# Performance work log

Hardware: AMD Instinct MI355X
Metric: run time of the kernel (lower is better)

Reference implementation:

```python
import jax, jax.numpy as jnp
import numpy as np

EPS = 1e-6

def _ln(x, g, b):
    m = jnp.mean(x, -1, keepdims=True)
    v = jnp.mean((x - m) ** 2, -1, keepdims=True)
    return (x - m) * jax.lax.rsqrt(v + 1e-5) * g + b

def _mha(qin, kin, vin, wq, bq, wk, bk, wv, bv, wo, bo, nh=8):
    B, T, D = qin.shape
    S = kin.shape[1]
    dh = D // nh
    q = (qin @ wq + bq).reshape(B, T, nh, dh)
    k = (kin @ wk + bk).reshape(B, S, nh, dh)
    v = (vin @ wv + bv).reshape(B, S, nh, dh)
    a = jax.nn.softmax(jnp.einsum('bthd,bshd->bhts', q, k) / np.float32(np.sqrt(dh)), -1)
    o = jnp.einsum('bhts,bshd->bthd', a, v).reshape(B, T, D)
    return o @ wo + bo

def _sinu_pe(pos, num_feats=128, temperature=20.0):
    # pos: [..., 2] (x, y); returns [..., 2*num_feats] ordered (y-feats, x-feats)
    dim_t = temperature ** ((2 * (jnp.arange(num_feats) // 2)) / num_feats)
    e = pos[..., None] * (2 * np.pi) / dim_t  # [..., 2, F]
    e = jnp.stack([jnp.sin(e[..., 0::2]), jnp.cos(e[..., 1::2])], -1).reshape(e.shape)
    return jnp.concatenate([e[..., 1, :], e[..., 0, :]], -1)

def _spatial36(b1, b2, sizes):
    # b1, b2: [B, Q, 4]; sizes: [B, 2] = (h, w). UPT-style 18 feats + log -> 36.
    h = sizes[:, 0:1]; w = sizes[:, 1:2]
    c1x = (b1[..., 0] + b1[..., 2]) / 2; c1y = (b1[..., 1] + b1[..., 3]) / 2
    c2x = (b2[..., 0] + b2[..., 2]) / 2; c2y = (b2[..., 1] + b2[..., 3]) / 2
    w1 = b1[..., 2] - b1[..., 0]; h1 = b1[..., 3] - b1[..., 1]
    w2 = b2[..., 2] - b2[..., 0]; h2 = b2[..., 3] - b2[..., 1]
    a1 = w1 * h1; a2 = w2 * h2
    dx = jnp.abs(c2x - c1x) / (w1 + EPS)
    dy = jnp.abs(c2y - c1y) / (h1 + EPS)
    ix = jnp.clip(jnp.minimum(b1[..., 2], b2[..., 2]) - jnp.maximum(b1[..., 0], b2[..., 0]), 0)
    iy = jnp.clip(jnp.minimum(b1[..., 3], b2[..., 3]) - jnp.maximum(b1[..., 1], b2[..., 1]), 0)
    inter = ix * iy
    iou = inter / (a1 + a2 - inter + EPS)
    f = jnp.stack([c1x / w, c1y / h, c2x / w, c2y / h, w1 / w, h1 / h, w2 / w, h2 / h,
                   a1 / (h * w), a2 / (h * w), a2 / (a1 + EPS), w1 / (h1 + EPS), w2 / (h2 + EPS), iou,
                   (c2x > c1x) * dx, (c2x < c1x) * dx, (c2y > c1y) * dy, (c2y < c1y) * dy], -1)
    return jnp.concatenate([f, jnp.log(f + EPS)], -1)

def _forward(boxes, embeds, image_sizes, pose, line, sw1, sb1, sw2, sb2, sw3, sb3, bw, bb, pw, pb, lw, lb, enc_pe_w, enc_pe_b, enc_qkv_w, enc_qkv_b, enc_out_w, enc_out_b, enc_ff1_w, enc_ff1_b, enc_ff2_w, enc_ff2_b, enc_ln1_g, enc_ln1_b, enc_ln2_g, enc_ln2_b, dec_q_w, dec_q_b, dec_kv_w, dec_kv_b, dec_out_w, dec_out_b, dec_ff1_w, dec_ff1_b, dec_ff2_w, dec_ff2_b, dec_ln1_g, dec_ln1_b, dec_ln2_g, dec_ln2_b, fc1_w, fc1_b, fc2_w, fc2_b, mln1_g, mln1_b, mln2_g, mln2_b, m1_w, m1_b, m2_w, m2_b, labels, nh):
    B, N, _ = boxes.shape
    # static human-object pairing (x != y) & (x < nh)
    xg, yg = np.meshgrid(np.arange(N), np.arange(N), indexing='ij')
    keep = (xg != yg) & (xg < nh)
    xk = jnp.asarray(xg[keep]); yk = jnp.asarray(yg[keep])  # [P]
    # line features: adaptive-avg-pool(1,1) + 1x1 conv == spatial mean + linear
    line_feat = jnp.mean(line, axis=(2, 3)) @ lw + lb  # [B, 256]
    # spatial head on all N*N ordered pairs, then gather kept pairs
    xa = jnp.asarray(xg.reshape(-1)); ya = jnp.asarray(yg.reshape(-1))
    f36 = _spatial36(boxes[:, xa], boxes[:, ya], image_sizes)  # [B, N*N, 36]
    s = jax.nn.relu(f36 @ sw1 + sb1)
    s = jax.nn.relu(s @ sw2 + sb2)
    s = jax.nn.relu(s @ sw3 + sb3)
    spa = s.reshape(B, N, N, -1)[:, xk, yk]  # [B, P, R]
    # box sinusoidal positional encodings (cat of centre-PE and wh-PE)
    whwh = image_sizes[:, jnp.array([1, 0, 1, 0])][:, None]  # [B,1,4]
    bxn = boxes / whwh
    ctr = (bxn[..., :2] + bxn[..., 2:]) / 2
    whb = bxn[..., 2:] - bxn[..., :2]
    box_pe = jnp.concatenate([_sinu_pe(ctr), _sinu_pe(whb)], -1)  # [B, N, 512]
    # 2-layer transformer encoder over instance tokens (pos added to q,k)
    posx = box_pe @ enc_pe_w + enc_pe_b
    x = embeds
    for i in range(enc_qkv_w.shape[0]):
        wq, wk_, wv = jnp.split(enc_qkv_w[i], 3, axis=1)
        bq, bk_, bv = jnp.split(enc_qkv_b[i], 3)
        qk = x + posx
        att = _mha(qk, qk, x, wq, bq, wk_, bk_, wv, bv, enc_out_w[i], enc_out_b[i])
        x = _ln(x + att, enc_ln1_g[i], enc_ln1_b[i])
        ff = jax.nn.relu(x @ enc_ff1_w[i] + enc_ff1_b[i]) @ enc_ff2_w[i] + enc_ff2_b[i]
        x = _ln(x + ff, enc_ln2_g[i], enc_ln2_b[i])
    # pair gather + human/object positional embeds (box PE projected + line feature)
    pe_h = box_pe[:, xk] @ bw + bb + line_feat[:, None, :]
    pe_o = box_pe[:, yk] @ bw + bb + line_feat[:, None, :]
    h = x[:, xk]; o = x[:, yk]  # [B, P, 256]
    pose_ctx = pose @ pw + pb  # [B, M, 256]
    # HO refine decoder: cross-attention from pair tokens to pose tokens
    for l in range(dec_q_w.shape[0]):
        wk_, wv = jnp.split(dec_kv_w[l], 2, axis=1)
        bk_, bv = jnp.split(dec_kv_b[l], 2)
        def _layer(feat, pe):
            att = _mha(feat + pe, pose_ctx, pose_ctx, dec_q_w[l], dec_q_b[l], wk_, bk_, wv, bv, dec_out_w[l], dec_out_b[l])
            feat = _ln(feat + att, dec_ln1_g[l], dec_ln1_b[l])
            ff = jax.nn.relu(feat @ dec_ff1_w[l] + dec_ff1_b[l]) @ dec_ff2_w[l] + dec_ff2_b[l]
            return _ln(feat + ff, dec_ln2_g[l], dec_ln2_b[l])
        h = _layer(h, pe_h)
        o = _layer(o, pe_o)
    # multi-modal fusion
    ho = jnp.concatenate([h, o], -1)  # [B, P, 512]
    ho = _ln(ho @ fc1_w + fc1_b, mln1_g, mln1_b)
    sp = _ln(spa @ fc2_w + fc2_b, mln2_g, mln2_b)
    z = jax.nn.relu(jnp.concatenate([ho, sp], -1))
    z = jax.nn.relu(z @ m1_w + m1_b)
    z = jax.nn.relu(z @ m2_w + m2_b)
    return z  # [B, P, 256] HOI query features

def setup_inputs() -> dict:
    key = jax.random.key(0)
    ks = iter(jax.random.split(key, 80))
    B, N, NH, M, HH, WW = 16, 128, 32, 64, 8, 8
    W = 0.05
    def rn(shape, s=1.0):
        return jax.random.normal(next(ks), shape, dtype=jnp.float32) * s
    def ru(shape):
        return jax.random.uniform(next(ks), shape, dtype=jnp.float32)
    sizes = 800.0 + 480.0 * ru((B, 2))  # (h, w)
    wh = sizes[:, jnp.array([1, 0])]
    xy = ru((B, N, 2)) * wh[:, None] * 0.7
    bwh = ru((B, N, 2)) * wh[:, None] * 0.25 + 4.0
    boxes = jnp.concatenate([xy, xy + bwh], -1)
    labels = jnp.concatenate([jnp.zeros((B, NH), jnp.int32), jax.random.randint(next(ks), (B, N - NH), 1, 81, dtype=jnp.int32)], -1)
    return dict(
        boxes=boxes, embeds=rn((B, N, 256)), image_sizes=sizes, pose=rn((B, M, 768)), line=rn((B, 2048, HH, WW)),
        sw1=rn((36, 128), W), sb1=jnp.zeros((128,)), sw2=rn((128, 256), W), sb2=jnp.zeros((256,)), sw3=rn((256, 256), W), sb3=jnp.zeros((256,)),
        bw=rn((512, 256), W), bb=jnp.zeros((256,)), pw=rn((768, 256), W), pb=jnp.zeros((256,)), lw=rn((2048, 256), W), lb=jnp.zeros((256,)),
        enc_pe_w=rn((512, 256), W), enc_pe_b=jnp.zeros((256,)),
        enc_qkv_w=rn((2, 256, 768), W), enc_qkv_b=jnp.zeros((2, 768)), enc_out_w=rn((2, 256, 256), W), enc_out_b=jnp.zeros((2, 256)),
        enc_ff1_w=rn((2, 256, 1024), W), enc_ff1_b=jnp.zeros((2, 1024)), enc_ff2_w=rn((2, 1024, 256), W), enc_ff2_b=jnp.zeros((2, 256)),
        enc_ln1_g=jnp.ones((2, 256)), enc_ln1_b=jnp.zeros((2, 256)), enc_ln2_g=jnp.ones((2, 256)), enc_ln2_b=jnp.zeros((2, 256)),
        dec_q_w=rn((2, 256, 256), W), dec_q_b=jnp.zeros((2, 256)), dec_kv_w=rn((2, 256, 512), W), dec_kv_b=jnp.zeros((2, 512)),
        dec_out_w=rn((2, 256, 256), W), dec_out_b=jnp.zeros((2, 256)),
        dec_ff1_w=rn((2, 256, 1024), W), dec_ff1_b=jnp.zeros((2, 1024)), dec_ff2_w=rn((2, 1024, 256), W), dec_ff2_b=jnp.zeros((2, 256)),
        dec_ln1_g=jnp.ones((2, 256)), dec_ln1_b=jnp.zeros((2, 256)), dec_ln2_g=jnp.ones((2, 256)), dec_ln2_b=jnp.zeros((2, 256)),
        fc1_w=rn((512, 256), W), fc1_b=jnp.zeros((256,)), fc2_w=rn((256, 256), W), fc2_b=jnp.zeros((256,)),
        mln1_g=jnp.ones((256,)), mln1_b=jnp.zeros((256,)), mln2_g=jnp.ones((256,)), mln2_b=jnp.zeros((256,)),
        m1_w=rn((512, 384), W), m1_b=jnp.zeros((384,)), m2_w=rn((384, 256), W), m2_b=jnp.zeros((256,)),
        labels=labels, nh=NH)

def reference(boxes, embeds, image_sizes, pose, line, sw1, sb1, sw2, sb2, sw3, sb3, bw, bb, pw, pb, lw, lb, enc_pe_w, enc_pe_b, enc_qkv_w, enc_qkv_b, enc_out_w, enc_out_b, enc_ff1_w, enc_ff1_b, enc_ff2_w, enc_ff2_b, enc_ln1_g, enc_ln1_b, enc_ln2_g, enc_ln2_b, dec_q_w, dec_q_b, dec_kv_w, dec_kv_b, dec_out_w, dec_out_b, dec_ff1_w, dec_ff1_b, dec_ff2_w, dec_ff2_b, dec_ln1_g, dec_ln1_b, dec_ln2_g, dec_ln2_b, fc1_w, fc1_b, fc2_w, fc2_b, mln1_g, mln1_b, mln2_g, mln2_b, m1_w, m1_b, m2_w, m2_b, labels, nh):
    return _forward(boxes, embeds, image_sizes, pose, line, sw1, sb1, sw2, sb2, sw3, sb3, bw, bb, pw, pb, lw, lb, enc_pe_w, enc_pe_b, enc_qkv_w, enc_qkv_b, enc_out_w, enc_out_b, enc_ff1_w, enc_ff1_b, enc_ff2_w, enc_ff2_b, enc_ln1_g, enc_ln1_b, enc_ln2_g, enc_ln2_b, dec_q_w, dec_q_b, dec_kv_w, dec_kv_b, dec_out_w, dec_out_b, dec_ff1_w, dec_ff1_b, dec_ff2_w, dec_ff2_b, dec_ln1_g, dec_ln1_b, dec_ln2_g, dec_ln2_b, fc1_w, fc1_b, fc2_w, fc2_b, mln1_g, mln1_b, mln2_g, mln2_b, m1_w, m1_b, m2_w, m2_b, labels, nh)
```

## Files before the change

kernel.cpp:

```cpp
#include <hip/hip_runtime.h>
#include <stdint.h>

static constexpr int B      = 16;
static constexpr int N      = 128;
static constexpr int P      = 4064;
static constexpr int MPOSE  = 64;
static constexpr int64_t BN = (int64_t)B * N;
static constexpr int64_t BP = (int64_t)B * P;

#define TWO_PI 6.283185307179586f
#define QSCALE 0.17677669529663687f

typedef __attribute__((ext_vector_type(4))) float f32x4;
typedef __attribute__((ext_vector_type(8))) short bf16x8;
typedef __attribute__((ext_vector_type(8))) unsigned short u16x8;
typedef __attribute__((ext_vector_type(4))) unsigned short u16x4;

__device__ __forceinline__ unsigned short f2bf(float f) {
    union { float f; unsigned u; } v; v.f = f;
    unsigned r = (v.u + 0x7fffu + ((v.u >> 16) & 1u)) >> 16;
    return (unsigned short)r;
}
__device__ __forceinline__ float bf2f(unsigned short u) {
    union { unsigned u; float f; } v; v.u = (unsigned)u << 16;
    return v.f;
}
__device__ __forceinline__ void pair_xy(int p, int& x, int& y) {
    x = p / 127;
    int r = p - x * 127;
    y = (r < x) ? r : r + 1;
}
__device__ __forceinline__ int xcd_swz(int orig, int nwg) {
    int q = nwg >> 3, r = nwg & 7;
    int xcd = orig & 7, idx = orig >> 3;
    return (xcd < r ? xcd * (q + 1) : r * (q + 1) + (xcd - r) * q) + idx;
}
__device__ __forceinline__ void gld16(const unsigned short* g, unsigned short* l) {
    __builtin_amdgcn_global_load_lds(
        (const __attribute__((address_space(1))) void*)g,
        (__attribute__((address_space(3))) void*)l, 16, 0, 0);
}

struct WDesc { const float* src; int64_t dstOff; int K, Nn, Kpad, blockStart; };
struct WTable { WDesc d[29]; int nDesc; };

__global__ __launch_bounds__(256) void wprep_all_k(WTable t, unsigned short* __restrict__ wt)
{
    __shared__ float s[32][33];
    int bid = blockIdx.x;
    int di = 0;
    for (int i = 1; i < t.nDesc; ++i) if (t.d[i].blockStart <= bid) di = i;
    const WDesc& d = t.d[di];
    int lbid = bid - d.blockStart;
    int kTiles = d.Kpad >> 5;
    int k0 = (lbid % kTiles) * 32, n0 = (lbid / kTiles) * 32;
    int tx = threadIdx.x & 31, ty = threadIdx.x >> 5;
#pragma unroll
    for (int i = 0; i < 4; ++i) {
        int k = k0 + ty + i * 8;
        s[ty + i * 8][tx] = (k < d.K) ? d.src[(int64_t)k * d.Nn + n0 + tx] : 0.f;
    }
    __syncthreads();
    unsigned short* dst = wt + d.dstOff;
#pragma unroll
    for (int i = 0; i < 4; ++i) {
        int n = n0 + ty + i * 8;
        dst[(int64_t)n * d.Kpad + k0 + tx] = f2bf(s[tx][ty + i * 8]);
    }
}

template <bool RELU_OUT>
__global__ __launch_bounds__(256) void bgemm_k(
    const float* __restrict__ A, const float* __restrict__ A2, int lda,
    const unsigned short* __restrict__ Bt, int ldk,
    const float* __restrict__ bias,
    const float* __restrict__ Cadd, int addStride, int addCols,
    const float* __restrict__ lfp,
    float* __restrict__ C, int ldc,
    int kSteps)
{
    __shared__ unsigned short As[128][40];
    __shared__ unsigned short Bs[128][40];
    const int tid  = threadIdx.x;
    const int lane = tid & 63;
    const int wave = tid >> 6;
    const int wr = wave >> 1, wc = wave & 1;
    const int row0 = blockIdx.y * 128, col0 = blockIdx.x * 128;
    const int l15 = lane & 15, l4 = lane >> 4;
    const int sr = tid >> 1;
    const int sh = (tid & 1) * 16;

    f32x4 acc[4][4] = {};

    for (int ks = 0; ks < kSteps; ++ks) {
        const int k0 = ks * 32;
        {
            const int64_t off = (int64_t)(row0 + sr) * lda + k0 + sh;
            const float* ap = A + off;
            float v[16];
#pragma unroll
            for (int i = 0; i < 4; ++i) {
                float4 tv = ((const float4*)ap)[i];
                v[i*4+0] = tv.x; v[i*4+1] = tv.y; v[i*4+2] = tv.z; v[i*4+3] = tv.w;
            }
            if (A2) {
                const float* ap2 = A2 + off;
#pragma unroll
                for (int i = 0; i < 4; ++i) {
                    float4 tv = ((const float4*)ap2)[i];
                    v[i*4+0] += tv.x; v[i*4+1] += tv.y; v[i*4+2] += tv.z; v[i*4+3] += tv.w;
                }
            }
            u16x8 p0, p1;
#pragma unroll
            for (int j = 0; j < 8; ++j) { p0[j] = f2bf(v[j]); p1[j] = f2bf(v[8 + j]); }
            *(u16x8*)&As[sr][sh]     = p0;
            *(u16x8*)&As[sr][sh + 8] = p1;
        }
        {
            const unsigned short* bp = Bt + (int64_t)(col0 + sr) * ldk + k0 + sh;
            *(u16x8*)&Bs[sr][sh]     = *(const u16x8*)bp;
            *(u16x8*)&Bs[sr][sh + 8] = *(const u16x8*)(bp + 8);
        }
        __syncthreads();
        bf16x8 af[4], bfr[4];
#pragma unroll
        for (int f = 0; f < 4; ++f) {
            af[f]  = *(const bf16x8*)&As[wr * 64 + f * 16 + l15][l4 * 8];
            bfr[f] = *(const bf16x8*)&Bs[wc * 64 + f * 16 + l15][l4 * 8];
        }
#pragma unroll
        for (int i = 0; i < 4; ++i)
#pragma unroll
            for (int j = 0; j < 4; ++j)
                acc[i][j] = __builtin_amdgcn_mfma_f32_16x16x32_bf16(af[i], bfr[j], acc[i][j], 0, 0, 0);
        __syncthreads();
    }
#pragma unroll
    for (int i = 0; i < 4; ++i) {
        int rb = row0 + wr * 64 + i * 16 + l4 * 4;
#pragma unroll
        for (int j = 0; j < 4; ++j) {
            int c = col0 + wc * 64 + j * 16 + l15;
            float bv = bias ? bias[c] : 0.f;
#pragma unroll
            for (int e = 0; e < 4; ++e) {
                int r = rb + e;
                float vv = acc[i][j][e] + bv;
                if (Cadd && c < addCols) vv += Cadd[(int64_t)r * addStride + c];
                if (lfp) vv += lfp[(r >> 7) * 256 + c];
                if (RELU_OUT) vv = fmaxf(vv, 0.f);
                C[(int64_t)r * ldc + c] = vv;
            }
        }
    }
}

static void bgemm(hipStream_t st,
                  const float* A, const float* A2, int lda,
                  const unsigned short* Bt, int ldk, const float* bias,
                  const float* Cadd, int addStride, int addCols, const float* lfp,
                  float* C, int ldc, int M, int Ncols, int K, bool reluOut)
{
    dim3 g(Ncols / 128, M / 128), b(256);
    if (reluOut) bgemm_k<true><<<g,b,0,st>>>(A,A2,lda,Bt,ldk,bias,Cadd,addStride,addCols,lfp,C,ldc,K/32);
    else         bgemm_k<false><<<g,b,0,st>>>(A,A2,lda,Bt,ldk,bias,Cadd,addStride,addCols,lfp,C,ldc,K/32);
}

__global__ __launch_bounds__(256) void tgemm16_k(
    const float* __restrict__ A, int lda,
    const unsigned short* __restrict__ Bt, int ldk,
    const float* __restrict__ bias,
    const float* __restrict__ res,
    const float* __restrict__ g, const float* __restrict__ be,
    float* __restrict__ C, int kSteps)
{
    __shared__ unsigned short As[16][40];
    __shared__ unsigned short Bs[256][40];
    __shared__ float partS[16][4], partQ[16][4];
    __shared__ float statM[16], statI[16];
    const int tid = threadIdx.x;
    const int lane = tid & 63, w = tid >> 6;
    const int l15 = lane & 15, l4 = lane >> 4;
    const int row0 = blockIdx.x * 16;

    f32x4 acc[4] = {};
    for (int ks = 0; ks < kSteps; ++ks) {
        int k0 = ks * 32;
        if (tid < 64) {
            const float* ap = A + (int64_t)(row0 + (tid >> 2)) * lda + k0 + (tid & 3) * 8;
            float4 t0 = ((const float4*)ap)[0];
            float4 t1 = ((const float4*)ap)[1];
            u16x8 p;
            p[0]=f2bf(t0.x); p[1]=f2bf(t0.y); p[2]=f2bf(t0.z); p[3]=f2bf(t0.w);
            p[4]=f2bf(t1.x); p[5]=f2bf(t1.y); p[6]=f2bf(t1.z); p[7]=f2bf(t1.w);
            *(u16x8*)&As[tid >> 2][(tid & 3) * 8] = p;
        }
        {
            const unsigned short* bp = Bt + (int64_t)tid * ldk + k0;
#pragma unroll
            for (int q = 0; q < 4; ++q)
                *(u16x8*)&Bs[tid][q * 8] = *(const u16x8*)(bp + q * 8);
        }
        __syncthreads();
        bf16x8 af = *(const bf16x8*)&As[l15][l4 * 8];
        bf16x8 bfr[4];
#pragma unroll
        for (int f = 0; f < 4; ++f)
            bfr[f] = *(const bf16x8*)&Bs[w * 64 + f * 16 + l15][l4 * 8];
#pragma unroll
        for (int j = 0; j < 4; ++j)
            acc[j] = __builtin_amdgcn_mfma_f32_16x16x32_bf16(af, bfr[j], acc[j], 0, 0, 0);
        __syncthreads();
    }
    float ps[4] = {}, pq[4] = {};
#pragma unroll
    for (int j = 0; j < 4; ++j) {
        int c = w * 64 + j * 16 + l15;
#pragma unroll
        for (int e = 0; e < 4; ++e) {
            int r = l4 * 4 + e;
            float v = acc[j][e] + bias[c] + res[(int64_t)(row0 + r) * 256 + c];
            acc[j][e] = v;
            ps[e] += v;
            pq[e] += v * v;
        }
    }
#pragma unroll
    for (int e = 0; e < 4; ++e) {
#pragma unroll
        for (int m = 1; m < 16; m <<= 1) {
            ps[e] += __shfl_xor(ps[e], m);
            pq[e] += __shfl_xor(pq[e], m);
        }
    }
    if (l15 == 0) {
#pragma unroll
        for (int e = 0; e < 4; ++e) {
            int r = l4 * 4 + e;
            partS[r][w] = ps[e];
            partQ[r][w] = pq[e];
        }
    }
    __syncthreads();
    if (tid < 16) {
        float s = partS[tid][0] + partS[tid][1] + partS[tid][2] + partS[tid][3];
        float q = partQ[tid][0] + partQ[tid][1] + partQ[tid][2] + partQ[tid][3];
        float m = s * (1.f/256.f);
        float var = q * (1.f/256.f) - m * m;
        statM[tid] = m;
        statI[tid] = rsqrtf(var + 1e-5f);
    }
    __syncthreads();
#pragma unroll
    for (int j = 0; j < 4; ++j) {
        int c = w * 64 + j * 16 + l15;
#pragma unroll
        for (int e = 0; e < 4; ++e) {
            int r = l4 * 4 + e;
            C[(int64_t)(row0 + r) * 256 + c] = (acc[j][e] - statM[r]) * statI[r] * g[c] + be[c];
        }
    }
}

template <bool RELU_OUT, bool OUT_BF16>
__global__ __launch_bounds__(256) void hgemm_k(
    const unsigned short* __restrict__ A, int lda,
    const unsigned short* __restrict__ Bt, int ldk,
    const float* __restrict__ bias,
    void* __restrict__ Cv, int ldc,
    int kSteps, int nx)
{
    __shared__ unsigned short As[128][32];
    __shared__ unsigned short Bs[128][32];
    const int tid  = threadIdx.x;
    const int lane = tid & 63;
    const int wave = tid >> 6;
    const int wr = wave >> 1, wc = wave & 1;
    const int wgid = xcd_swz(blockIdx.x, gridDim.x);
    const int row0 = (wgid / nx) * 128, col0 = (wgid % nx) * 128;
    const int l15 = lane & 15, l4 = lane >> 4;
    const int srow = lane >> 2;
    const int scol = (lane & 3) * 8;

    f32x4 acc[4][4] = {};
    for (int ks = 0; ks < kSteps; ++ks) {
        const int k0 = ks * 32;
#pragma unroll
        for (int i = 0; i < 2; ++i) {
            int seg = wave * 2 + i;
            int r = seg * 16 + srow;
            gld16(A  + (int64_t)(row0 + r) * lda + k0 + scol, &As[seg * 16][0]);
            gld16(Bt + (int64_t)(col0 + r) * ldk + k0 + scol, &Bs[seg * 16][0]);
        }
        __syncthreads();
        bf16x8 af[4], bfr[4];
#pragma unroll
        for (int f = 0; f < 4; ++f) {
            af[f]  = *(const bf16x8*)&As[wr * 64 + f * 16 + l15][l4 * 8];
            bfr[f] = *(const bf16x8*)&Bs[wc * 64 + f * 16 + l15][l4 * 8];
        }
#pragma unroll
        for (int i = 0; i < 4; ++i)
#pragma unroll
            for (int j = 0; j < 4; ++j)
                acc[i][j] = __builtin_amdgcn_mfma_f32_16x16x32_bf16(af[i], bfr[j], acc[i][j], 0, 0, 0);
        __syncthreads();
    }
#pragma unroll
    for (int i = 0; i < 4; ++i) {
        int rb = row0 + wr * 64 + i * 16 + l4 * 4;
#pragma unroll
        for (int j = 0; j < 4; ++j) {
            int c = col0 + wc * 64 + j * 16 + l15;
            float bv = bias ? bias[c] : 0.f;
#pragma unroll
            for (int e = 0; e < 4; ++e) {
                int64_t off = (int64_t)(rb + e) * ldc + c;
                float vv = acc[i][j][e] + bv;
                if (RELU_OUT) vv = fmaxf(vv, 0.f);
                if (OUT_BF16) ((unsigned short*)Cv)[off] = f2bf(vv);
                else          ((float*)Cv)[off] = vv;
            }
        }
    }
}

__global__ __launch_bounds__(256) void spa_k(
    const float* __restrict__ boxes, const float* __restrict__ sizes,
    const unsigned short* __restrict__ W1, const float* __restrict__ b1,
    const unsigned short* __restrict__ W2, const float* __restrict__ b2,
    unsigned short* __restrict__ t3out, int chunk0)
{
    __shared__ unsigned short F[128][72];
    __shared__ unsigned short Bs[128][40];
    __shared__ unsigned short D1s[128][136];
    const int tid  = threadIdx.x;
    const int lane = tid & 63;
    const int wave = tid >> 6;
    const int wr = wave >> 1, wc = wave & 1;
    const int row0 = blockIdx.x * 128;
    const int l15 = lane & 15, l4 = lane >> 4;
    const int sr = tid >> 1;
    const int sh = (tid & 1) * 16;

    if (tid < 128) {
        int gp = chunk0 + row0 + tid;
        int b = gp / P, p = gp - b * P;
        int xi, yi; pair_xy(p, xi, yi);
        const float* b1x = boxes + ((int64_t)b * N + xi) * 4;
        const float* b2x = boxes + ((int64_t)b * N + yi) * 4;
        float h = sizes[b * 2 + 0], w = sizes[b * 2 + 1];
        float c1x = (b1x[0] + b1x[2]) * 0.5f, c1y = (b1x[1] + b1x[3]) * 0.5f;
        float c2x = (b2x[0] + b2x[2]) * 0.5f, c2y = (b2x[1] + b2x[3]) * 0.5f;
        float w1 = b1x[2] - b1x[0], h1 = b1x[3] - b1x[1];
        float w2 = b2x[2] - b2x[0], h2 = b2x[3] - b2x[1];
        float a1 = w1 * h1, a2 = w2 * h2;
        float dx = fabsf(c2x - c1x) / (w1 + 1e-6f);
        float dy = fabsf(c2y - c1y) / (h1 + 1e-6f);
        float ix = fmaxf(fminf(b1x[2], b2x[2]) - fmaxf(b1x[0], b2x[0]), 0.f);
        float iy = fmaxf(fminf(b1x[3], b2x[3]) - fmaxf(b1x[1], b2x[1]), 0.f);
        float inter = ix * iy;
        float iou = inter / (a1 + a2 - inter + 1e-6f);
        float f[18];
        f[0] = c1x / w;  f[1] = c1y / h;  f[2] = c2x / w;  f[3] = c2y / h;
        f[4] = w1 / w;   f[5] = h1 / h;   f[6] = w2 / w;   f[7] = h2 / h;
        f[8] = a1 / (h * w); f[9] = a2 / (h * w); f[10] = a2 / (a1 + 1e-6f);
        f[11] = w1 / (h1 + 1e-6f); f[12] = w2 / (h2 + 1e-6f); f[13] = iou;
        f[14] = (c2x > c1x) ? dx : 0.f;  f[15] = (c2x < c1x) ? dx : 0.f;
        f[16] = (c2y > c1y) ? dy : 0.f;  f[17] = (c2y < c1y) ? dy : 0.f;
#pragma unroll
        for (int i = 0; i < 18; ++i) {
            F[tid][i]      = f2bf(f[i]);
            F[tid][18 + i] = f2bf(logf(f[i] + 1e-6f));
        }
#pragma unroll
        for (int i = 36; i < 64; ++i) F[tid][i] = 0;
    }
    __syncthreads();

    f32x4 acc1[4][4] = {};
    for (int ks = 0; ks < 2; ++ks) {
        const int k0 = ks * 32;
        {
            const unsigned short* bp = W1 + (int64_t)sr * 64 + k0 + sh;
            *(u16x8*)&Bs[sr][sh]     = *(const u16x8*)bp;
            *(u16x8*)&Bs[sr][sh + 8] = *(const u16x8*)(bp + 8);
        }
        __syncthreads();
        bf16x8 af[4], bfr[4];
#pragma unroll
        for (int f = 0; f < 4; ++f) {
            af[f]  = *(const bf16x8*)&F[wr * 64 + f * 16 + l15][k0 + l4 * 8];
            bfr[f] = *(const bf16x8*)&Bs[wc * 64 + f * 16 + l15][l4 * 8];
        }
#pragma unroll
        for (int i = 0; i < 4; ++i)
#pragma unroll
            for (int j = 0; j < 4; ++j)
                acc1[i][j] = __builtin_amdgcn_mfma_f32_16x16x32_bf16(af[i], bfr[j], acc1[i][j], 0, 0, 0);
        __syncthreads();
    }
#pragma unroll
    for (int i = 0; i < 4; ++i) {
        int rb = wr * 64 + i * 16 + l4 * 4;
#pragma unroll
        for (int j = 0; j < 4; ++j) {
            int c = wc * 64 + j * 16 + l15;
            float bv = b1[c];
#pragma unroll
            for (int e = 0; e < 4; ++e)
                D1s[rb + e][c] = f2bf(fmaxf(acc1[i][j][e] + bv, 0.f));
        }
    }
    __syncthreads();

    f32x4 acc2[2][4][4] = {};
#pragma unroll
    for (int n = 0; n < 2; ++n) {
        for (int kk = 0; kk < 4; ++kk) {
            {
                const unsigned short* bp = W2 + (int64_t)(n * 128 + sr) * 128 + kk * 32 + sh;
                *(u16x8*)&Bs[sr][sh]     = *(const u16x8*)bp;
                *(u16x8*)&Bs[sr][sh + 8] = *(const u16x8*)(bp + 8);
            }
            __syncthreads();
            bf16x8 af[4], bfr[4];
#pragma unroll
            for (int f = 0; f < 4; ++f) {
                af[f]  = *(const bf16x8*)&D1s[wr * 64 + f * 16 + l15][kk * 32 + l4 * 8];
                bfr[f] = *(const bf16x8*)&Bs[wc * 64 + f * 16 + l15][l4 * 8];
            }
#pragma unroll
            for (int i = 0; i < 4; ++i)
#pragma unroll
                for (int j = 0; j < 4; ++j)
                    acc2[n][i][j] = __builtin_amdgcn_mfma_f32_16x16x32_bf16(af[i], bfr[j], acc2[n][i][j], 0, 0, 0);
            __syncthreads();
        }
    }
#pragma unroll
    for (int n = 0; n < 2; ++n)
#pragma unroll
    for (int i = 0; i < 4; ++i) {
        int rb = row0 + wr * 64 + i * 16 + l4 * 4;
#pragma unroll
        for (int j = 0; j < 4; ++j) {
            int c = n * 128 + wc * 64 + j * 16 + l15;
            float bv = b2[c];
#pragma unroll
            for (int e = 0; e < 4; ++e)
                t3out[(int64_t)(rb + e) * 256 + c] = f2bf(fmaxf(acc2[n][i][j][e] + bv, 0.f));
        }
    }
}

__global__ __launch_bounds__(256) void zprep_k(
    const float* __restrict__ UV, const float* __restrict__ fb,
    const unsigned short* __restrict__ t3,
    const float* __restrict__ g1, const float* __restrict__ be1,
    const float* __restrict__ g2, const float* __restrict__ be2,
    unsigned short* __restrict__ zb, int chunk0, int rows)
{
    int wave = threadIdx.x >> 6, lane = threadIdx.x & 63;
    int li = blockIdx.x * 4 + wave;
    if (li >= rows) return;
    int gp = chunk0 + li;
    int b = gp / P, p = gp - b * P;
    int xi, yi; pair_xy(p, xi, yi);
    int c = lane * 4;
    {
        float4 u  = *(const float4*)(UV + ((int64_t)(b * 128 + xi)) * 512 + c);
        float4 vv = *(const float4*)(UV + ((int64_t)(b * 128 + yi)) * 512 + 256 + c);
        float4 fbv = *(const float4*)(fb + c);
        float4 v;
        v.x = u.x + vv.x + fbv.x; v.y = u.y + vv.y + fbv.y;
        v.z = u.z + vv.z + fbv.z; v.w = u.w + vv.w + fbv.w;
        float s  = v.x + v.y + v.z + v.w;
        float sq = v.x*v.x + v.y*v.y + v.z*v.z + v.w*v.w;
#pragma unroll
        for (int off = 1; off < 64; off <<= 1) {
            s  += __shfl_xor(s, off);
            sq += __shfl_xor(sq, off);
        }
        float m = s * (1.f/256.f);
        float var = sq * (1.f/256.f) - m * m;
        float inv = rsqrtf(var + 1e-5f);
        float4 gg = *(const float4*)(g1 + c);
        float4 bb = *(const float4*)(be1 + c);
        u16x4 o;
        o[0] = f2bf(fmaxf((v.x - m) * inv * gg.x + bb.x, 0.f));
        o[1] = f2bf(fmaxf((v.y - m) * inv * gg.y + bb.y, 0.f));
        o[2] = f2bf(fmaxf((v.z - m) * inv * gg.z + bb.z, 0.f));
        o[3] = f2bf(fmaxf((v.w - m) * inv * gg.w + bb.w, 0.f));
        *(u16x4*)(zb + (int64_t)li * 512 + c) = o;
    }
    {
        u16x4 u = *(const u16x4*)(t3 + (int64_t)li * 256 + c);
        float4 v;
        v.x = bf2f(u[0]); v.y = bf2f(u[1]); v.z = bf2f(u[2]); v.w = bf2f(u[3]);
        float s  = v.x + v.y + v.z + v.w;
        float sq = v.x*v.x + v.y*v.y + v.z*v.z + v.w*v.w;
#pragma unroll
        for (int off = 1; off < 64; off <<= 1) {
            s  += __shfl_xor(s, off);
            sq += __shfl_xor(sq, off);
        }
        float m = s * (1.f/256.f);
        float var = sq * (1.f/256.f) - m * m;
        float inv = rsqrtf(var + 1e-5f);
        float4 gg = *(const float4*)(g2 + c);
        float4 bb = *(const float4*)(be2 + c);
        u16x4 o;
        o[0] = f2bf(fmaxf((v.x - m) * inv * gg.x + bb.x, 0.f));
        o[1] = f2bf(fmaxf((v.y - m) * inv * gg.y + bb.y, 0.f));
        o[2] = f2bf(fmaxf((v.z - m) * inv * gg.z + bb.z, 0.f));
        o[3] = f2bf(fmaxf((v.w - m) * inv * gg.w + bb.w, 0.f));
        *(u16x4*)(zb + (int64_t)li * 512 + 256 + c) = o;
    }
}

__global__ __launch_bounds__(256) void line_mean_k(const float* __restrict__ line, float* __restrict__ lm)
{
    int wave = threadIdx.x >> 6, lane = threadIdx.x & 63;
    int bc = blockIdx.x * 4 + wave;
    float v = line[(int64_t)bc * 64 + lane];
#pragma unroll
    for (int off = 1; off < 64; off <<= 1) v += __shfl_xor(v, off);
    if (lane == 0) lm[bc] = v * (1.f/64.f);
}

__global__ __launch_bounds__(256) void line_proj_k(
    const float* __restrict__ lm, const float* __restrict__ lw,
    const float* __restrict__ lb, float* __restrict__ lf)
{
    __shared__ float red[8][32];
    int b = blockIdx.y, jg = blockIdx.x;
    int jj = threadIdx.x & 31, cc = threadIdx.x >> 5;
    int j = jg * 32 + jj;
    const float* lmb = lm + (int64_t)b * 2048 + cc * 256;
    const float* lwp = lw + (int64_t)(cc * 256) * 256 + j;
    float acc = 0.f;
#pragma unroll 4
    for (int k = 0; k < 256; ++k) acc += lmb[k] * lwp[(int64_t)k * 256];
    red[cc][jj] = acc;
    __syncthreads();
    if (cc == 0) {
        float s = lb[j];
#pragma unroll
        for (int i = 0; i < 8; ++i) s += red[i][jj];
        lf[b * 256 + j] = s;
    }
}

__global__ __launch_bounds__(512) void boxpe_k(
    const float* __restrict__ boxes, const float* __restrict__ sizes, float* __restrict__ boxpe)
{
    int row = blockIdx.x;
    int b = row >> 7;
    int i = threadIdx.x;
    const float* bx = boxes + (int64_t)row * 4;
    float h = sizes[b * 2 + 0], w = sizes[b * 2 + 1];
    float x0 = bx[0] / w, y0 = bx[1] / h, x1 = bx[2] / w, y1 = bx[3] / h;
    int seg = i >> 7, j = i & 127, k = j >> 1;
    float val;
    switch (seg) {
        case 0: val = (y0 + y1) * 0.5f; break;
        case 1: val = (x0 + x1) * 0.5f; break;
        case 2: val = (y1 - y0); break;
        default: val = (x1 - x0); break;
    }
    float dimt = exp2f((float)k * (4.321928094887362f / 64.f));
    float arg = val * TWO_PI / dimt;
    boxpe[(int64_t)row * 512 + i] = (j & 1) ? cosf(arg) : sinf(arg);
}

__global__ __launch_bounds__(128) void enc_attn_k(
    const float* __restrict__ qkv, float* __restrict__ outp)
{
    int b = blockIdx.x >> 3, hd = blockIdx.x & 7;
    __shared__ float kl[128][32];
    __shared__ float vl[128][32];
    int tid = threadIdx.x;
    for (int i = tid; i < 128 * 32; i += 128) {
        int s = i >> 5, j = i & 31;
        const float* rp = qkv + ((int64_t)(b * 128 + s)) * 768 + hd * 32 + j;
        kl[s][j] = rp[256];
        vl[s][j] = rp[512];
    }
    __syncthreads();
    int t = tid;
    const float* qp = qkv + ((int64_t)(b * 128 + t)) * 768 + hd * 32;
    float qr[32];
#pragma unroll
    for (int j = 0; j < 32; ++j) qr[j] = qp[j] * QSCALE;
    float m = -1e30f, l = 0.f;
    for (int s = 0; s < 128; ++s) {
        float d = 0.f;
#pragma unroll
        for (int j = 0; j < 32; ++j) d += qr[j] * kl[s][j];
        float mn = fmaxf(m, d);
        l = l * __expf(m - mn) + __expf(d - mn);
        m = mn;
    }
    float acc[32] = {};
    for (int s = 0; s < 128; ++s) {
        float d = 0.f;
#pragma unroll
        for (int j = 0; j < 32; ++j) d += qr[j] * kl[s][j];
        float wgt = __expf(d - m);
#pragma unroll
        for (int j = 0; j < 32; ++j) acc[j] += wgt * vl[s][j];
    }
    float linv = 1.f / l;
    float* op = outp + ((int64_t)(b * 128 + t)) * 256 + hd * 32;
#pragma unroll
    for (int j = 0; j < 32; ++j) op[j] = acc[j] * linv;
}

__global__ __launch_bounds__(256) void dec_attn_k(
    const float* __restrict__ q, const float* __restrict__ kv, int ldkv,
    float* __restrict__ outp, int rows, int rpb)
{
    int hd = blockIdx.y;
    int r0 = blockIdx.x * 256;
    __shared__ float kl[2][64][32];
    __shared__ float vl[2][64][32];
    int tid = threadIdx.x;
    int b0 = r0 / rpb;
    int b1 = (r0 + 255) / rpb;
    if (b1 >= B) b1 = B - 1;
    for (int i = tid; i < 64 * 32; i += 256) {
        int s = i >> 5, j = i & 31;
        int64_t off0 = ((int64_t)(b0 * MPOSE + s)) * ldkv + hd * 32 + j;
        int64_t off1 = ((int64_t)(b1 * MPOSE + s)) * ldkv + hd * 32 + j;
        kl[0][s][j] = kv[off0];
        vl[0][s][j] = kv[off0 + 256];
        kl[1][s][j] = kv[off1];
        vl[1][s][j] = kv[off1 + 256];
    }
    __syncthreads();
    int r = r0 + tid;
    if (r >= rows) return;
    int which = (r / rpb == b0) ? 0 : 1;
    int64_t qoff = (int64_t)r * 256 + hd * 32;
    float qr[32];
#pragma unroll
    for (int j = 0; j < 32; ++j) qr[j] = q[qoff + j] * QSCALE;
    float m = -1e30f, l = 0.f;
    for (int s = 0; s < 64; ++s) {
        float d = 0.f;
#pragma unroll
        for (int j = 0; j < 32; ++j) d += qr[j] * kl[which][s][j];
        float mn = fmaxf(m, d);
        l = l * __expf(m - mn) + __expf(d - mn);
        m = mn;
    }
    float acc[32] = {};
    for (int s = 0; s < 64; ++s) {
        float d = 0.f;
#pragma unroll
        for (int j = 0; j < 32; ++j) d += qr[j] * kl[which][s][j];
        float wgt = __expf(d - m);
#pragma unroll
        for (int j = 0; j < 32; ++j) acc[j] += wgt * vl[which][s][j];
    }
    float linv = 1.f / l;
#pragma unroll
    for (int j = 0; j < 32; ++j) outp[qoff + j] = acc[j] * linv;
}

static constexpr int64_t WT_QKV  = 0;
static constexpr int64_t WT_EOUT = WT_QKV  + 2*196608;
static constexpr int64_t WT_EFF1 = WT_EOUT + 2*65536;
static constexpr int64_t WT_EFF2 = WT_EFF1 + 2*262144;
static constexpr int64_t WT_DQ   = WT_EFF2 + 2*262144;
static constexpr int64_t WT_DKV  = WT_DQ   + 2*65536;
static constexpr int64_t WT_DOUT = WT_DKV  + 2*131072;
static constexpr int64_t WT_DFF1 = WT_DOUT + 2*65536;
static constexpr int64_t WT_DFF2 = WT_DFF1 + 2*262144;
static constexpr int64_t WT_SW1  = WT_DFF2 + 2*262144;
static constexpr int64_t WT_SW2  = WT_SW1 + 8192;
static constexpr int64_t WT_SW3  = WT_SW2 + 32768;
static constexpr int64_t WT_BW   = WT_SW3 + 65536;
static constexpr int64_t WT_PW   = WT_BW  + 131072;
static constexpr int64_t WT_EPE  = WT_PW  + 196608;
static constexpr int64_t WT_FC1  = WT_EPE + 131072;
static constexpr int64_t WT_FC2  = WT_FC1 + 131072;
static constexpr int64_t WT_M1   = WT_FC2 + 65536;
static constexpr int64_t WT_M2   = WT_M1  + 196608;
static constexpr int64_t WT_TOTAL = WT_M2 + 98304;

extern "C" void kernel_launch(void* const* d_in, const int* in_sizes, int n_in,
                              void* d_out, int out_size, void* d_ws, size_t ws_size,
                              hipStream_t stream)
{
    (void)in_sizes; (void)n_in; (void)out_size;
    const float* boxes     = (const float*)d_in[0];
    const float* embeds    = (const float*)d_in[1];
    const float* sizes     = (const float*)d_in[2];
    const float* pose      = (const float*)d_in[3];
    const float* line      = (const float*)d_in[4];
    const float* sw1 = (const float*)d_in[5];  const float* sb1 = (const float*)d_in[6];
    const float* sw2 = (const float*)d_in[7];  const float* sb2 = (const float*)d_in[8];
    const float* sw3 = (const float*)d_in[9];  const float* sb3 = (const float*)d_in[10];
    const float* bw  = (const float*)d_in[11]; const float* bb  = (const float*)d_in[12];
    const float* pw  = (const float*)d_in[13]; const float* pb  = (const float*)d_in[14];
    const float* lw  = (const float*)d_in[15]; const float* lb  = (const float*)d_in[16];
    const float* enc_pe_w  = (const float*)d_in[17]; const float* enc_pe_b = (const float*)d_in[18];
    const float* enc_qkv_w = (const float*)d_in[19]; const float* enc_qkv_b = (const float*)d_in[20];
    const float* enc_out_w = (const float*)d_in[21]; const float* enc_out_b = (const float*)d_in[22];
    const float* enc_ff1_w = (const float*)d_in[23]; const float* enc_ff1_b = (const float*)d_in[24];
    const float* enc_ff2_w = (const float*)d_in[25]; const float* enc_ff2_b = (const float*)d_in[26];
    const float* enc_ln1_g = (const float*)d_in[27]; const float* enc_ln1_b = (const float*)d_in[28];
    const float* enc_ln2_g = (const float*)d_in[29]; const float* enc_ln2_b = (const float*)d_in[30];
    const float* dec_q_w   = (const float*)d_in[31]; const float* dec_q_b  = (const float*)d_in[32];
    const float* dec_kv_w  = (const float*)d_in[33]; const float* dec_kv_b = (const float*)d_in[34];
    const float* dec_out_w = (const float*)d_in[35]; const float* dec_out_b = (const float*)d_in[36];
    const float* dec_ff1_w = (const float*)d_in[37]; const float* dec_ff1_b = (const float*)d_in[38];
    const float* dec_ff2_w = (const float*)d_in[39]; const float* dec_ff2_b = (const float*)d_in[40];
    const float* dec_ln1_g = (const float*)d_in[41]; const float* dec_ln1_b = (const float*)d_in[42];
    const float* dec_ln2_g = (const float*)d_in[43]; const float* dec_ln2_b = (const float*)d_in[44];
    const float* fc1_w = (const float*)d_in[45]; const float* fc1_b = (const float*)d_in[46];
    const float* fc2_w = (const float*)d_in[47]; const float* fc2_b = (const float*)d_in[48];
    const float* mln1_g = (const float*)d_in[49]; const float* mln1_b = (const float*)d_in[50];
    const float* mln2_g = (const float*)d_in[51]; const float* mln2_b = (const float*)d_in[52];
    const float* m1_w = (const float*)d_in[53]; const float* m1_b = (const float*)d_in[54];
    const float* m2_w = (const float*)d_in[55]; const float* m2_b = (const float*)d_in[56];
    float* out = (float*)d_out;

    float* base = (float*)d_ws;
    int64_t wsf = (int64_t)(ws_size / sizeof(float));
    float* x_   = base;
    float* bpw_ = x_   + 524288;
    float* lf   = bpw_ + 524288;
    float* kv0  = lf   + 4096;
    unsigned short* wt = (unsigned short*)(kv0 + 1048576);
    float* arena = (float*)(wt + WT_TOTAL);
    const int64_t LIVE_F = arena - base;
    int64_t arena_f = wsf - LIVE_F;
    if (arena_f < 0) arena_f = 0;

    float* posx  = arena;
    float* boxpe = posx  + 524288;
    float* pqkv  = boxpe + 1048576;
    float* e_qkv = pqkv  + 3145728;
    float* e_t   = e_qkv + 1572864;
    float* e_ff  = e_t   + 524288;
    float* pctx  = e_ff  + 2097152;
    float* lm    = pctx  + 262144;

    int64_t rc = ((arena_f * 2) / 1152) & ~127LL;
    if (rc > BP) rc = BP;
    if (rc < 128) rc = 128;

    {
        WTable T;
        int nd = 0, bs = 0;
        auto add = [&](const float* src, int64_t dstOff, int K, int Nn, int Kpad) {
            T.d[nd] = { src, dstOff, K, Nn, Kpad, bs };
            bs += (Kpad / 32) * (Nn / 32);
            ++nd;
        };
        for (int i = 0; i < 2; ++i) {
            add(enc_qkv_w + (int64_t)i*196608, WT_QKV  + i*196608, 256, 768, 256);
            add(enc_out_w + (int64_t)i*65536,  WT_EOUT + i*65536,  256, 256, 256);
            add(enc_ff1_w + (int64_t)i*262144, WT_EFF1 + i*262144, 256, 1024, 256);
            add(enc_ff2_w + (int64_t)i*262144, WT_EFF2 + i*262144, 1024, 256, 1024);
            add(dec_q_w   + (int64_t)i*65536,  WT_DQ   + i*65536,  256, 256, 256);
            add(dec_kv_w  + (int64_t)i*131072, WT_DKV  + i*131072, 256, 512, 256);
            add(dec_out_w + (int64_t)i*65536,  WT_DOUT + i*65536,  256, 256, 256);
            add(dec_ff1_w + (int64_t)i*262144, WT_DFF1 + i*262144, 256, 1024, 256);
            add(dec_ff2_w + (int64_t)i*262144, WT_DFF2 + i*262144, 1024, 256, 1024);
        }
        add(sw1, WT_SW1, 36, 128, 64);
        add(sw2, WT_SW2, 128, 256, 128);
        add(sw3, WT_SW3, 256, 256, 256);
        add(bw,  WT_BW,  512, 256, 512);
        add(pw,  WT_PW,  768, 256, 768);
        add(enc_pe_w, WT_EPE, 512, 256, 512);
        add(fc1_w,             WT_FC1,         256, 256, 256);
        add(fc1_w + 256 * 256, WT_FC1 + 65536, 256, 256, 256);
        add(fc2_w, WT_FC2, 256, 256, 256);
        add(m1_w, WT_M1, 512, 384, 512);
        add(m2_w, WT_M2, 384, 256, 384);
        T.nDesc = nd;
        wprep_all_k<<<bs, 256, 0, stream>>>(T, wt);
    }

    line_mean_k<<<8192, 256, 0, stream>>>(line, lm);
    line_proj_k<<<dim3(8, B), 256, 0, stream>>>(lm, lw, lb, lf);
    boxpe_k<<<(int)BN, 512, 0, stream>>>(boxes, sizes, boxpe);
    bgemm(stream, boxpe, nullptr, 512, wt + WT_EPE, 512, enc_pe_b, nullptr, 0, 0, nullptr,
          posx, 256, (int)BN, 256, 512, false);
    bgemm(stream, boxpe, nullptr, 512, wt + WT_BW,  512, bb, nullptr, 0, 0, lf,
          bpw_, 256, (int)BN, 256, 512, false);
    bgemm(stream, pose,  nullptr, 768, wt + WT_PW,  768, pb, nullptr, 0, 0, nullptr,
          pctx, 256, B*MPOSE, 256, 768, false);
    bgemm(stream, pctx, nullptr, 256, wt + WT_DKV, 256, dec_kv_b, nullptr, 0, 0, nullptr,
          kv0, 1024, B*MPOSE, 1024, 256, false);
    bgemm(stream, posx, nullptr, 256, wt + WT_QKV, 256, nullptr, nullptr, 0, 0, nullptr,
          pqkv, 1536, (int)BN, 1536, 256, false);

    for (int i = 0; i < 2; ++i) {
        const float* xin = (i == 0) ? embeds : x_;
        const unsigned short* Wq = wt + WT_QKV + (int64_t)i * 196608;
        bgemm(stream, xin, nullptr, 256, Wq, 256, enc_qkv_b + (int64_t)i*768,
              pqkv + i*768, 1536, 512, nullptr, e_qkv, 768, (int)BN, 768, 256, false);
        enc_attn_k<<<B * 8, 128, 0, stream>>>(e_qkv, e_t);
        tgemm16_k<<<(int)(BN / 16), 256, 0, stream>>>(e_t, 256, wt + WT_EOUT + (int64_t)i*65536, 256,
            enc_out_b + i*256, xin, enc_ln1_g + i*256, enc_ln1_b + i*256, x_, 8);
        bgemm(stream, x_, nullptr, 256, wt + WT_EFF1 + (int64_t)i*262144, 256, enc_ff1_b + i*1024,
              nullptr, 0, 0, nullptr, e_ff, 1024, (int)BN, 1024, 256, true);
        tgemm16_k<<<(int)(BN / 16), 256, 0, stream>>>(e_ff, 1024, wt + WT_EFF2 + (int64_t)i*262144, 1024,
            enc_ff2_b + i*256, x_, enc_ln2_g + i*256, enc_ln2_b + i*256, x_, 32);
    }

    for (int l = 0; l < 2; ++l) {
        bgemm(stream, x_, bpw_, 256, wt + WT_DQ + (int64_t)l*65536, 256, dec_q_b + l*256,
              nullptr, 0, 0, nullptr, e_t, 256, (int)BN, 256, 256, false);
        dec_attn_k<<<dim3((int)(BN / 256), 8), 256, 0, stream>>>(e_t, kv0 + l*512, 1024, e_qkv, (int)BN, N);
        tgemm16_k<<<(int)(BN / 16), 256, 0, stream>>>(e_qkv, 256, wt + WT_DOUT + (int64_t)l*65536, 256,
            dec_out_b + l*256, x_, dec_ln1_g + l*256, dec_ln1_b + l*256, x_, 8);
        bgemm(stream, x_, nullptr, 256, wt + WT_DFF1 + (int64_t)l*262144, 256, dec_ff1_b + l*1024,
              nullptr, 0, 0, nullptr, e_ff, 1024, (int)BN, 1024, 256, true);
        tgemm16_k<<<(int)(BN / 16), 256, 0, stream>>>(e_ff, 1024, wt + WT_DFF2 + (int64_t)l*262144, 1024,
            dec_ff2_b + l*256, x_, dec_ln2_g + l*256, dec_ln2_b + l*256, x_, 32);
    }
    float* UV = kv0;
    bgemm(stream, x_, nullptr, 256, wt + WT_FC1, 256, nullptr, nullptr, 0, 0, nullptr,
          UV, 512, (int)BN, 512, 256, false);

    for (int64_t c0 = 0; c0 < BP; c0 += rc) {
        int rows = (int)((BP - c0 < rc) ? (BP - c0) : rc);
        unsigned short* t3 = (unsigned short*)arena;
        unsigned short* zb = t3 + (int64_t)rc * 256;
        unsigned short* z2 = zb + (int64_t)rc * 512;

        spa_k<<<rows / 128, 256, 0, stream>>>(boxes, sizes,
            wt + WT_SW1, sb1, wt + WT_SW2, sb2, t3, (int)c0);
        hgemm_k<true,true><<<2 * (rows / 128), 256, 0, stream>>>(
            t3, 256, wt + WT_SW3, 256, sb3, z2, 256, 8, 2);
        hgemm_k<false,true><<<2 * (rows / 128), 256, 0, stream>>>(
            z2, 256, wt + WT_FC2, 256, fc2_b, t3, 256, 8, 2);
        zprep_k<<<rows / 4, 256, 0, stream>>>(UV, fc1_b, t3, mln1_g, mln1_b, mln2_g, mln2_b,
                                              zb, (int)c0, rows);
        hgemm_k<true,true><<<3 * (rows / 128), 256, 0, stream>>>(
            zb, 512, wt + WT_M1, 512, m1_b, z2, 384, 16, 3);
        hgemm_k<true,false><<<2 * (rows / 128), 256, 0, stream>>>(
            z2, 384, wt + WT_M2, 384, m2_b, out + c0 * 256, 256, 12, 2);
    }
}
```

Baseline: 814.0 us.

## Double-buffer LDS tiles in hgemm_k to overlap global loads with MFMA

The generic bf16 GEMM kernel now keeps two LDS buffers for the A and B tiles and prefetches the next k-step's tiles with direct-to-LDS loads while the MFMAs run on the current buffer. It replaces the two __syncthreads per step with one explicit vmcnt wait plus barrier. This hides global-load latency behind compute, at the cost of doubling LDS use per block, which may reduce occupancy. The GEMM is only one of several kernels in the forward pass, so the end-to-end effect depends on its share of the total time.

```diff
diff --git a/kernel.cpp b/kernel.cpp
--- a/kernel.cpp
+++ b/kernel.cpp
@@ -271,8 +271,8 @@
     void* __restrict__ Cv, int ldc,
     int kSteps, int nx)
 {
-    __shared__ unsigned short As[128][32];
-    __shared__ unsigned short Bs[128][32];
+    __shared__ unsigned short As[2][128][32];
+    __shared__ unsigned short Bs[2][128][32];
     const int tid  = threadIdx.x;
     const int lane = tid & 63;
     const int wave = tid >> 6;
@@ -284,28 +284,49 @@
     const int scol = (lane & 3) * 8;
 
     f32x4 acc[4][4] = {};
-    for (int ks = 0; ks < kSteps; ++ks) {
-        const int k0 = ks * 32;
+
+    {
+        const int k0 = 0;
 #pragma unroll
         for (int i = 0; i < 2; ++i) {
             int seg = wave * 2 + i;
             int r = seg * 16 + srow;
-            gld16(A  + (int64_t)(row0 + r) * lda + k0 + scol, &As[seg * 16][0]);
-            gld16(Bt + (int64_t)(col0 + r) * ldk + k0 + scol, &Bs[seg * 16][0]);
-        }
-        __syncthreads();
+            gld16(A  + (int64_t)(row0 + r) * lda + k0 + scol, &As[0][seg * 16][0]);
+            gld16(Bt + (int64_t)(col0 + r) * ldk + k0 + scol, &Bs[0][seg * 16][0]);
+        }
+    }
+    asm volatile("s_waitcnt vmcnt(0)" ::: "memory");
+    __builtin_amdgcn_s_barrier();
+    asm volatile("" ::: "memory");
+
+    int cur = 0;
+    for (int ks = 0; ks < kSteps; ++ks) {
+        if (ks + 1 < kSteps) {
+            const int k0n = (ks + 1) * 32;
+            const int nb = cur ^ 1;
+#pragma unroll
+            for (int i = 0; i < 2; ++i) {
+                int seg = wave * 2 + i;
+                int r = seg * 16 + srow;
+                gld16(A  + (int64_t)(row0 + r) * lda + k0n + scol, &As[nb][seg * 16][0]);
+                gld16(Bt + (int64_t)(col0 + r) * ldk + k0n + scol, &Bs[nb][seg * 16][0]);
+            }
+        }
         bf16x8 af[4], bfr[4];
 #pragma unroll
         for (int f = 0; f < 4; ++f) {
-            af[f]  = *(const bf16x8*)&As[wr * 64 + f * 16 + l15][l4 * 8];
-            bfr[f] = *(const bf16x8*)&Bs[wc * 64 + f * 16 + l15][l4 * 8];
+            af[f]  = *(const bf16x8*)&As[cur][wr * 64 + f * 16 + l15][l4 * 8];
+            bfr[f] = *(const bf16x8*)&Bs[cur][wc * 64 + f * 16 + l15][l4 * 8];
         }
 #pragma unroll
         for (int i = 0; i < 4; ++i)
 #pragma unroll
             for (int j = 0; j < 4; ++j)
                 acc[i][j] = __builtin_amdgcn_mfma_f32_16x16x32_bf16(af[i], bfr[j], acc[i][j], 0, 0, 0);
-        __syncthreads();
+        asm volatile("s_waitcnt vmcnt(0)" ::: "memory");
+        __builtin_amdgcn_s_barrier();
+        asm volatile("" ::: "memory");
+        cur ^= 1;
     }
 #pragma unroll
     for (int i = 0; i < 4; ++i) {
```

New measurement: 795.8 us. 2.2% less time.
